# Kernel optimization log

Measured on AMD Instinct MI355X. Metric: run time of the kernel, lower is better.

Reference implementation:

```python
import jax, jax.numpy as jnp
import numpy as np

B, V, H = 4, 256, 128
EPS = 1e-5


def setup_inputs() -> dict:
    key = jax.random.key(0)
    ks = jax.random.split(key, 16)
    inp = {
        "h1": jax.random.normal(ks[0], (B, V, H), jnp.float32),
        "h2": jax.random.normal(ks[1], (B, V, H), jnp.float32),
        "e": jax.random.normal(ks[2], (B, V, V, H), jnp.float32),
        "graph": jax.random.randint(ks[3], (B, V, V), 0, 2, jnp.int32),
    }
    scale = 1.0 / np.sqrt(H)
    for i, nm in enumerate(["U1", "U2", "V1", "V2", "A1", "A2", "C"]):
        inp[f"W_{nm}"] = jax.random.normal(ks[4 + i], (H, H), jnp.float32) * scale
        inp[f"b_{nm}"] = jnp.zeros((H,), jnp.float32)
    for nm in ["h1", "h2", "e"]:
        inp[f"g_{nm}"] = jnp.ones((H,), jnp.float32)   # BN gamma
        inp[f"be_{nm}"] = jnp.zeros((H,), jnp.float32)  # BN beta
    return inp


def _lin(x, W, b):
    # torch nn.Linear: x @ W.T + b
    return jnp.einsum('...i,oi->...o', x, W) + b


def _bn(x, g, b):
    # BatchNorm1d with track_running_stats=False: batch stats over flattened leading dims
    sh = x.shape
    x2 = x.reshape(-1, sh[-1])
    m = x2.mean(axis=0)
    v = x2.var(axis=0)  # biased, as torch BN uses for normalization
    return ((x2 - m) * jax.lax.rsqrt(v + EPS) * g + b).reshape(sh)


def reference(h1, h2, e, graph,
              W_U1, b_U1, W_U2, b_U2, W_V1, b_V1, W_V2, b_V2,
              W_A1, b_A1, W_A2, b_A2, W_C, b_C,
              g_h1, be_h1, g_h2, be_h2, g_e, be_e):
    h1_in, h2_in, e_in = h1, h2, e

    Uh1 = _lin(h1, W_U1, b_U1)
    Uh2 = _lin(h2, W_U2, b_U2)
    Vh1 = _lin(h1, W_V1, b_V1)
    Vh2 = _lin(h2, W_V2, b_V2)

    # Wh1[b,i,j,h] = Vh1[b,j,h] + Vh2[b,i,h] ; Wh2 = transpose(1,2) pattern
    Wh1 = Vh1[:, None, :, :] + Vh2[:, :, None, :]
    Wh2 = Vh1[:, :, None, :] + Vh2[:, None, :, :]

    Ah1 = _lin(h1, W_A1, b_A1)
    Ah2 = _lin(h2, W_A2, b_A2)
    Ce = _lin(e, W_C, b_C)
    e_new = Ah1[:, None, :, :] + Ah2[:, :, None, :] + Ce  # B x V x V x H

    gates = jax.nn.sigmoid(e_new)
    gates_T = jax.nn.sigmoid(jnp.transpose(e_new, (0, 2, 1, 3)))

    # aggregation = 'sum' over dim 2 (graph unused for sum)
    h1n = Uh1 + jnp.sum(gates * Wh1, axis=2)
    h2n = Uh2 + jnp.sum(gates_T * Wh2, axis=2)

    h1n = jax.nn.relu(_bn(h1n, g_h1, be_h1))
    h2n = jax.nn.relu(_bn(h2n, g_h2, be_h2))
    e_out = jax.nn.relu(_bn(e_new, g_e, be_e))

    # mode == 'residual'
    return (h1_in + h1n, h2_in + h2n, e_in + e_out)
```

## Files before the change

### kernel.cpp

```cpp
#include <hip/hip_runtime.h>
#include <math.h>

#define BB 4
#define VV 256
#define HH 128
#define EPS 1e-5f

typedef __attribute__((ext_vector_type(8))) short short8;
typedef __attribute__((ext_vector_type(8))) __bf16 bf16x8;
typedef __attribute__((ext_vector_type(4))) float f32x4;

__device__ __forceinline__ float sigm_(float x) {
    return 1.0f / (1.0f + __expf(-x));
}

__device__ __forceinline__ bf16x8 as_bf(short8 s) {
    union { short8 s; bf16x8 b; } u; u.s = s; return u.b;
}

__device__ __forceinline__ void split8n(const float4 x0, const float4 x1,
                                        bf16x8& hi, bf16x8& lo) {
    float xs[8] = {x0.x, x0.y, x0.z, x0.w, x1.x, x1.y, x1.z, x1.w};
    #pragma unroll
    for (int i = 0; i < 8; ++i) {
        float x = xs[i];
        __bf16 h = (__bf16)x;
        float r = x - (float)h;
        hi[i] = h;
        lo[i] = (__bf16)r;
    }
}

__global__ __launch_bounds__(256) void k0_splitW(const float* __restrict__ W_C,
                                                 short* __restrict__ Whl) {
    int t = blockIdx.x * 256 + threadIdx.x;
    int lane = t & 63;
    int grp = t >> 6;
    int kstep = grp >> 3, nsub = grp & 7;
    int n = nsub * 16 + (lane & 15);
    int kb = kstep * 32 + ((lane >> 4) & 3) * 8;
    const float4* src = (const float4*)(W_C + (size_t)n * HH + kb);
    float4 x0 = src[0], x1 = src[1];
    bf16x8 hi, lo;
    split8n(x0, x1, hi, lo);
    union { bf16x8 b; short8 s; } uh, ul;
    uh.b = hi; ul.b = lo;
    short8* dst = (short8*)Whl;
    dst[(size_t)grp * 128 + 0 * 64 + lane] = uh.s;
    dst[(size_t)grp * 128 + 1 * 64 + lane] = ul.s;
}

struct LinArgs {
    const float* x1; const float* x2;
    const float* W[6]; const float* b[6]; const float* b2[6];
    float* out[6]; float* outf[6];
};

__global__ __launch_bounds__(128) void k1_linears(LinArgs a) {
    __shared__ float xs[2][8][HH];
    const int t = threadIdx.x;
    const int r0 = blockIdx.x * 8;
    {
        const float4* s1 = (const float4*)(a.x1 + (size_t)r0 * HH);
        const float4* s2 = (const float4*)(a.x2 + (size_t)r0 * HH);
        float4* d1 = (float4*)&xs[0][0][0];
        float4* d2 = (float4*)&xs[1][0][0];
        #pragma unroll
        for (int p = 0; p < 2; ++p) {
            d1[t + p * 128] = s1[t + p * 128];
            d2[t + p * 128] = s2[t + p * 128];
        }
    }
    __syncthreads();
    const int h = t;
    const int l15h = h & 15, nsh = h >> 4;
    for (int g = 0; g < 6; ++g) {
        const float* W = a.W[g];
        const float (*x)[HH] = (g < 3) ? xs[0] : xs[1];
        float acc[8];
        #pragma unroll
        for (int r = 0; r < 8; ++r) acc[r] = 0.f;
        const float4* Wrow = (const float4*)(W + (size_t)h * HH);
        #pragma unroll 8
        for (int kq = 0; kq < 32; ++kq) {
            float4 w4 = Wrow[kq];
            #pragma unroll
            for (int r = 0; r < 8; ++r) {
                float4 ev = *(const float4*)&x[r][kq * 4];
                acc[r] = fmaf(ev.x, w4.x, acc[r]);
                acc[r] = fmaf(ev.y, w4.y, acc[r]);
                acc[r] = fmaf(ev.z, w4.z, acc[r]);
                acc[r] = fmaf(ev.w, w4.w, acc[r]);
            }
        }
        float bias = a.b[g][h];
        if (a.b2[g]) bias += a.b2[g][h];
        if (a.out[g]) {
            float* O = a.out[g] + (size_t)r0 * HH + h;
            #pragma unroll
            for (int r = 0; r < 8; ++r) O[(size_t)r * HH] = acc[r] + bias;
        }
        if (a.outf[g]) {
            float* Of = a.outf[g];
            #pragma unroll
            for (int r = 0; r < 8; ++r)
                Of[((size_t)(r0 + r) * 16 + l15h) * 8 + nsh] = acc[r] + bias;
        }
    }
}

__global__ __launch_bounds__(512, 4) void k2_main(
    const float* __restrict__ e,
    const short* __restrict__ Whl,
    const float* __restrict__ A1f, const float* __restrict__ A2f,
    const float* __restrict__ V1f, const float* __restrict__ V2f,
    float* __restrict__ e_new,
    float* __restrict__ h1acc,
    float* __restrict__ stats)
{
    __shared__ short8 sW[4096];
    __shared__ float red[8][3][8][16];
    const int t = threadIdx.x;
    const int l = t & 63;
    const int w = t >> 6;
    const int l15 = l & 15;
    const int lq = (l >> 4) & 3;
    const int bi = blockIdx.x;
    const int b = bi >> 8;
    const int jbase = w * 32;

    {
        const short8* src = (const short8*)Whl;
        #pragma unroll
        for (int p = 0; p < 8; ++p) sW[p * 512 + t] = src[p * 512 + t];
    }
    __syncthreads();

    const float* ebase = e + (size_t)bi * (VV * HH);
    const float* pa = ebase + (size_t)(jbase + l15) * HH + lq * 8;

    f32x4 acc[2][8];
    #pragma unroll
    for (int js = 0; js < 2; ++js)
        #pragma unroll
        for (int ns = 0; ns < 8; ++ns)
            acc[js][ns] = (f32x4){0.f, 0.f, 0.f, 0.f};

    float4 ec0 = *(const float4*)(pa);
    float4 ec1 = *(const float4*)(pa + 4);
    float4 ec2 = *(const float4*)(pa + 16 * HH);
    float4 ec3 = *(const float4*)(pa + 16 * HH + 4);

    #pragma unroll
    for (int kstep = 0; kstep < 4; ++kstep) {
        bf16x8 ah[2], al[2];
        split8n(ec0, ec1, ah[0], al[0]);
        split8n(ec2, ec3, ah[1], al[1]);
        if (kstep < 3) {
            const float* pn = pa + (kstep + 1) * 32;
            ec0 = *(const float4*)(pn);
            ec1 = *(const float4*)(pn + 4);
            ec2 = *(const float4*)(pn + 16 * HH);
            ec3 = *(const float4*)(pn + 16 * HH + 4);
        }
        #pragma unroll
        for (int ns = 0; ns < 8; ++ns) {
            short8 bh = sW[(size_t)(kstep * 8 + ns) * 128 + l];
            short8 bl = sW[(size_t)(kstep * 8 + ns) * 128 + 64 + l];
            acc[0][ns] = __builtin_amdgcn_mfma_f32_16x16x32_bf16(
                ah[0], as_bf(bh), acc[0][ns], 0, 0, 0);
            acc[1][ns] = __builtin_amdgcn_mfma_f32_16x16x32_bf16(
                ah[1], as_bf(bh), acc[1][ns], 0, 0, 0);
            acc[0][ns] = __builtin_amdgcn_mfma_f32_16x16x32_bf16(
                ah[0], as_bf(bl), acc[0][ns], 0, 0, 0);
            acc[1][ns] = __builtin_amdgcn_mfma_f32_16x16x32_bf16(
                ah[1], as_bf(bl), acc[1][ns], 0, 0, 0);
            acc[0][ns] = __builtin_amdgcn_mfma_f32_16x16x32_bf16(
                al[0], as_bf(bh), acc[0][ns], 0, 0, 0);
            acc[1][ns] = __builtin_amdgcn_mfma_f32_16x16x32_bf16(
                al[1], as_bf(bh), acc[1][ns], 0, 0, 0);
        }
    }

    union f8u { float4 v[2]; float f[8]; };
    f8u a2, v2;
    {
        const float4* p = (const float4*)(A2f + ((size_t)bi * 16 + l15) * 8);
        a2.v[0] = p[0]; a2.v[1] = p[1];
        const float4* q = (const float4*)(V2f + ((size_t)bi * 16 + l15) * 8);
        v2.v[0] = q[0]; v2.v[1] = q[1];
    }
    float h1a[8], es[8], eq[8];
    #pragma unroll
    for (int ns = 0; ns < 8; ++ns) { h1a[ns] = 0.f; es[ns] = 0.f; eq[ns] = 0.f; }

    #pragma unroll
    for (int js = 0; js < 2; ++js) {
        #pragma unroll
        for (int r = 0; r < 4; ++r) {
            int j = jbase + js * 16 + lq * 4 + r;
            size_t fro = ((size_t)(b * VV + j) * 16 + l15) * 8;
            f8u a1, v1;
            {
                const float4* p = (const float4*)(A1f + fro);
                a1.v[0] = p[0]; a1.v[1] = p[1];
                const float4* q = (const float4*)(V1f + fro);
                v1.v[0] = q[0]; v1.v[1] = q[1];
            }
            size_t obase = ((size_t)bi * VV + j) * HH;
            #pragma unroll
            for (int ns = 0; ns < 8; ++ns) {
                float en = acc[js][ns][r] + a1.f[ns] + a2.f[ns];
                e_new[obase + ns * 16 + l15] = en;
                float s = sigm_(en);
                h1a[ns] = fmaf(s, v1.f[ns] + v2.f[ns], h1a[ns]);
                es[ns] += en;
                eq[ns] = fmaf(en, en, eq[ns]);
            }
        }
    }

    #pragma unroll
    for (int ns = 0; ns < 8; ++ns) {
        h1a[ns] += __shfl_xor(h1a[ns], 16);
        h1a[ns] += __shfl_xor(h1a[ns], 32);
        es[ns]  += __shfl_xor(es[ns], 16);
        es[ns]  += __shfl_xor(es[ns], 32);
        eq[ns]  += __shfl_xor(eq[ns], 16);
        eq[ns]  += __shfl_xor(eq[ns], 32);
    }
    if (l < 16) {
        #pragma unroll
        for (int ns = 0; ns < 8; ++ns) {
            red[w][0][ns][l15] = h1a[ns];
            red[w][1][ns][l15] = es[ns];
            red[w][2][ns][l15] = eq[ns];
        }
    }
    __syncthreads();
    if (t < 128) {
        int ns = t >> 4, li = t & 15;
        float h1t = 0.f, est = 0.f, eqt = 0.f;
        #pragma unroll
        for (int ww = 0; ww < 8; ++ww) {
            h1t += red[ww][0][ns][li];
            est += red[ww][1][ns][li];
            eqt += red[ww][2][ns][li];
        }
        int n = t;
        h1acc[(size_t)bi * HH + n] = h1t;
        atomicAdd(&stats[0 * HH + n], est);
        atomicAdd(&stats[1 * HH + n], eqt);
    }
}

__global__ __launch_bounds__(256) void k4_pass2(
    float* __restrict__ e_io,
    const float* __restrict__ e_in,
    const float* __restrict__ V1, const float* __restrict__ V2,
    const float* __restrict__ g_e, const float* __restrict__ be_e,
    float* __restrict__ h2acc,
    const float* __restrict__ stats)
{
    const int t = threadIdx.x;
    const int h4 = (t & 31) * 4;
    const int jsub = t >> 5;
    const int blk = blockIdx.x;
    const int Iq = blk & 7;
    const int Jt = (blk >> 3) & 31;
    const int b = blk >> 8;
    const int J = Jt * 8 + jsub;
    const int bJ = (b << 8) + J;

    const float inv_n = 1.0f / (float)(BB * VV * VV);
    float sc[4], sh[4];
    #pragma unroll
    for (int c = 0; c < 4; ++c) {
        int h = h4 + c;
        float mean = stats[0 * HH + h] * inv_n;
        float var  = stats[1 * HH + h] * inv_n - mean * mean;
        float rstd = rsqrtf(var + EPS);
        sc[c] = rstd * g_e[h];
        sh[c] = be_e[h] - mean * sc[c];
    }
    float4 vh1 = *(const float4*)(V1 + (size_t)bJ * HH + h4);
    float4 h2a = {0.f, 0.f, 0.f, 0.f};

    const int I0beg = Iq * 32;
    for (int I0 = I0beg; I0 < I0beg + 32; I0 += 4) {
        float4 en[4], ei[4], v2[4];
        size_t off[4];
        #pragma unroll
        for (int u = 0; u < 4; ++u) {
            int I = I0 + u;
            off[u] = ((size_t)((b * VV + I) * VV) + J) * HH + h4;
            en[u] = *(const float4*)(e_io + off[u]);
            ei[u] = *(const float4*)(e_in + off[u]);
            v2[u] = *(const float4*)(V2 + (size_t)((b << 8) + I) * HH + h4);
        }
        #pragma unroll
        for (int u = 0; u < 4; ++u) {
            float4 r;
            float* enf = (float*)&en[u];
            float* eif = (float*)&ei[u];
            float* v2f = (float*)&v2[u];
            float* rf = (float*)&r;
            float* h2f = (float*)&h2a;
            float* v1f = (float*)&vh1;
            #pragma unroll
            for (int c = 0; c < 4; ++c) {
                float e_ = enf[c];
                h2f[c] = fmaf(sigm_(e_), v1f[c] + v2f[c], h2f[c]);
                float bn = fmaf(e_, sc[c], sh[c]);
                rf[c] = eif[c] + fmaxf(bn, 0.f);
            }
            *(float4*)(e_io + off[u]) = r;
        }
    }
    float* base = h2acc + (size_t)bJ * HH + h4;
    float* h2f = (float*)&h2a;
    #pragma unroll
    for (int c = 0; c < 4; ++c) atomicAdd(base + c, h2f[c]);
}

__global__ __launch_bounds__(256) void k45_combine(
    float* __restrict__ h1acc, float* __restrict__ h2acc,
    const float* __restrict__ U1, const float* __restrict__ U2,
    float* __restrict__ stats)
{
    __shared__ float red[2][2][128];
    const int t = threadIdx.x;
    const int h = t & 127;
    const int rr = t >> 7;
    const int region = blockIdx.x >> 5;
    const int r0 = (blockIdx.x & 31) * 32;
    float* acc = region ? h2acc : h1acc;
    const float* U = region ? U2 : U1;
    float s = 0.f, q = 0.f;
    #pragma unroll
    for (int rs = 0; rs < 16; ++rs) {
        size_t idx = (size_t)(r0 + rr * 16 + rs) * HH + h;
        float v = acc[idx] + U[idx];
        acc[idx] = v;
        s += v;
        q = fmaf(v, v, q);
    }
    red[0][rr][h] = s;
    red[1][rr][h] = q;
    __syncthreads();
    if (t < 128) {
        atomicAdd(&stats[(2 + 2 * region) * HH + h], red[0][0][h] + red[0][1][h]);
        atomicAdd(&stats[(3 + 2 * region) * HH + h], red[1][0][h] + red[1][1][h]);
    }
}

__global__ __launch_bounds__(256) void k5_final(
    const float* __restrict__ h1_in, const float* __restrict__ h2_in,
    const float* __restrict__ h1p, const float* __restrict__ h2p,
    const float* __restrict__ g1, const float* __restrict__ be1,
    const float* __restrict__ g2, const float* __restrict__ be2,
    float* __restrict__ out,
    const float* __restrict__ stats)
{
    const float inv_n = 1.0f / 1024.0f;
    int idx0 = blockIdx.x * 2048 + threadIdx.x;
    #pragma unroll
    for (int p = 0; p < 8; ++p) {
        int idx = idx0 + p * 256;
        int region = idx >> 17;
        int local = idx & 131071;
        int h = idx & 127;
        float ssum = stats[(2 + 2 * region) * HH + h];
        float ssq  = stats[(3 + 2 * region) * HH + h];
        float mean = ssum * inv_n;
        float var  = ssq * inv_n - mean * mean;
        float rstd = rsqrtf(var + EPS);
        const float* g  = region ? g2 : g1;
        const float* be = region ? be2 : be1;
        float sc = rstd * g[h];
        float sh = be[h] - mean * sc;
        const float* xin = region ? h2_in : h1_in;
        const float* pre = region ? h2p : h1p;
        out[idx] = xin[local] + fmaxf(fmaf(pre[local], sc, sh), 0.f);
    }
}

extern "C" void kernel_launch(void* const* d_in, const int* in_sizes, int n_in,
                              void* d_out, int out_size, void* d_ws, size_t ws_size,
                              hipStream_t stream) {
    const float* h1   = (const float*)d_in[0];
    const float* h2   = (const float*)d_in[1];
    const float* e    = (const float*)d_in[2];
    const float* W_U1 = (const float*)d_in[4];
    const float* b_U1 = (const float*)d_in[5];
    const float* W_U2 = (const float*)d_in[6];
    const float* b_U2 = (const float*)d_in[7];
    const float* W_V1 = (const float*)d_in[8];
    const float* b_V1 = (const float*)d_in[9];
    const float* W_V2 = (const float*)d_in[10];
    const float* b_V2 = (const float*)d_in[11];
    const float* W_A1 = (const float*)d_in[12];
    const float* b_A1 = (const float*)d_in[13];
    const float* W_A2 = (const float*)d_in[14];
    const float* b_A2 = (const float*)d_in[15];
    const float* W_C  = (const float*)d_in[16];
    const float* b_C  = (const float*)d_in[17];
    const float* g_h1 = (const float*)d_in[18];
    const float* be_h1= (const float*)d_in[19];
    const float* g_h2 = (const float*)d_in[20];
    const float* be_h2= (const float*)d_in[21];
    const float* g_e  = (const float*)d_in[22];
    const float* be_e = (const float*)d_in[23];

    float* ws = (float*)d_ws;
    const size_t S = (size_t)BB * VV * HH;
    float* U1  = ws + 0 * S;
    float* U2  = ws + 1 * S;
    float* V1  = ws + 2 * S;
    float* V2  = ws + 3 * S;
    float* V1f = ws + 4 * S;
    float* V2f = ws + 5 * S;
    float* A1f = ws + 6 * S;
    float* A2f = ws + 7 * S;
    float* h1acc = ws + 8 * S;
    float* h2acc = ws + 9 * S;
    float* stats = ws + 10 * S;
    short* Whl  = (short*)(stats + 768);

    float* out = (float*)d_out;
    float* eo = out + 2 * S;

    hipMemsetAsync(h1acc, 0, (2 * S + 768) * sizeof(float), stream);

    k0_splitW<<<8, 256, 0, stream>>>(W_C, Whl);

    LinArgs la;
    la.x1 = h1; la.x2 = h2;
    la.W[0] = W_U1; la.b[0] = b_U1; la.b2[0] = nullptr; la.out[0] = U1; la.outf[0] = nullptr;
    la.W[1] = W_V1; la.b[1] = b_V1; la.b2[1] = nullptr; la.out[1] = V1; la.outf[1] = V1f;
    la.W[2] = W_A1; la.b[2] = b_A1; la.b2[2] = b_C;     la.out[2] = nullptr; la.outf[2] = A1f;
    la.W[3] = W_U2; la.b[3] = b_U2; la.b2[3] = nullptr; la.out[3] = U2; la.outf[3] = nullptr;
    la.W[4] = W_V2; la.b[4] = b_V2; la.b2[4] = nullptr; la.out[4] = V2; la.outf[4] = V2f;
    la.W[5] = W_A2; la.b[5] = b_A2; la.b2[5] = nullptr; la.out[5] = nullptr; la.outf[5] = A2f;
    k1_linears<<<128, 128, 0, stream>>>(la);

    k2_main<<<BB * VV, 512, 0, stream>>>(e, Whl, A1f, A2f, V1f, V2f,
                                         eo, h1acc, stats);

    k4_pass2<<<BB * 32 * 8, 256, 0, stream>>>(eo, e, V1, V2, g_e, be_e,
                                              h2acc, stats);

    k45_combine<<<64, 256, 0, stream>>>(h1acc, h2acc, U1, U2, stats);

    k5_final<<<128, 256, 0, stream>>>(h1, h2, h1acc, h2acc,
                                      g_h1, be_h1, g_h2, be_h2, out, stats);
}
```

Baseline: 200.3 us.

## Swap MFMA operand order for row-contiguous float4 e_new stores

Swaps the A/B operands of the bf16 MFMA so each lane's accumulator holds four consecutive H columns instead of four rows. The epilogue can then write e_new and read A1/V1 in row-major layout as float4 vectors, and the fragment-ordered copies V1f/V2f/A1f/A2f produced by the linear kernel are dropped. The reduction changes from cross-quadrant shuffles to 16-lane xor shuffles per column group, with a flat shared buffer. This cuts scattered scalar global stores and workspace traffic, at the cost of more shuffle steps and loop-varying register indexing.

Result: slower. 213.2 us (+6.5%).

```diff
diff --git a/kernel.cpp b/kernel.cpp
--- a/kernel.cpp
+++ b/kernel.cpp
@@ -53,7 +53,7 @@
 struct LinArgs {
     const float* x1; const float* x2;
     const float* W[6]; const float* b[6]; const float* b2[6];
-    float* out[6]; float* outf[6];
+    float* out[6];
 };
 
 __global__ __launch_bounds__(128) void k1_linears(LinArgs a) {
@@ -73,7 +73,6 @@
     }
     __syncthreads();
     const int h = t;
-    const int l15h = h & 15, nsh = h >> 4;
     for (int g = 0; g < 6; ++g) {
         const float* W = a.W[g];
         const float (*x)[HH] = (g < 3) ? xs[0] : xs[1];
@@ -95,31 +94,24 @@
         }
         float bias = a.b[g][h];
         if (a.b2[g]) bias += a.b2[g][h];
-        if (a.out[g]) {
-            float* O = a.out[g] + (size_t)r0 * HH + h;
-            #pragma unroll
-            for (int r = 0; r < 8; ++r) O[(size_t)r * HH] = acc[r] + bias;
-        }
-        if (a.outf[g]) {
-            float* Of = a.outf[g];
-            #pragma unroll
-            for (int r = 0; r < 8; ++r)
-                Of[((size_t)(r0 + r) * 16 + l15h) * 8 + nsh] = acc[r] + bias;
-        }
+        float* O = a.out[g] + (size_t)r0 * HH + h;
+        #pragma unroll
+        for (int r = 0; r < 8; ++r) O[(size_t)r * HH] = acc[r] + bias;
     }
 }
 
 __global__ __launch_bounds__(512, 4) void k2_main(
     const float* __restrict__ e,
     const short* __restrict__ Whl,
-    const float* __restrict__ A1f, const float* __restrict__ A2f,
-    const float* __restrict__ V1f, const float* __restrict__ V2f,
+    const float* __restrict__ A1b,
+    const float* __restrict__ A2,
+    const float* __restrict__ V1, const float* __restrict__ V2,
     float* __restrict__ e_new,
     float* __restrict__ h1acc,
     float* __restrict__ stats)
 {
     __shared__ short8 sW[4096];
-    __shared__ float red[8][3][8][16];
+    __shared__ float red[8][3][128];
     const int t = threadIdx.x;
     const int l = t & 63;
     const int w = t >> 6;
@@ -168,89 +160,81 @@
             short8 bh = sW[(size_t)(kstep * 8 + ns) * 128 + l];
             short8 bl = sW[(size_t)(kstep * 8 + ns) * 128 + 64 + l];
             acc[0][ns] = __builtin_amdgcn_mfma_f32_16x16x32_bf16(
-                ah[0], as_bf(bh), acc[0][ns], 0, 0, 0);
+                as_bf(bh), ah[0], acc[0][ns], 0, 0, 0);
             acc[1][ns] = __builtin_amdgcn_mfma_f32_16x16x32_bf16(
-                ah[1], as_bf(bh), acc[1][ns], 0, 0, 0);
+                as_bf(bh), ah[1], acc[1][ns], 0, 0, 0);
             acc[0][ns] = __builtin_amdgcn_mfma_f32_16x16x32_bf16(
-                ah[0], as_bf(bl), acc[0][ns], 0, 0, 0);
+                as_bf(bl), ah[0], acc[0][ns], 0, 0, 0);
             acc[1][ns] = __builtin_amdgcn_mfma_f32_16x16x32_bf16(
-                ah[1], as_bf(bl), acc[1][ns], 0, 0, 0);
+                as_bf(bl), ah[1], acc[1][ns], 0, 0, 0);
             acc[0][ns] = __builtin_amdgcn_mfma_f32_16x16x32_bf16(
-                al[0], as_bf(bh), acc[0][ns], 0, 0, 0);
+                as_bf(bh), al[0], acc[0][ns], 0, 0, 0);
             acc[1][ns] = __builtin_amdgcn_mfma_f32_16x16x32_bf16(
-                al[1], as_bf(bh), acc[1][ns], 0, 0, 0);
-        }
-    }
-
-    union f8u { float4 v[2]; float f[8]; };
-    f8u a2, v2;
-    {
-        const float4* p = (const float4*)(A2f + ((size_t)bi * 16 + l15) * 8);
-        a2.v[0] = p[0]; a2.v[1] = p[1];
-        const float4* q = (const float4*)(V2f + ((size_t)bi * 16 + l15) * 8);
-        v2.v[0] = q[0]; v2.v[1] = q[1];
-    }
-    float h1a[8], es[8], eq[8];
-    #pragma unroll
-    for (int ns = 0; ns < 8; ++ns) { h1a[ns] = 0.f; es[ns] = 0.f; eq[ns] = 0.f; }
-
-    #pragma unroll
-    for (int js = 0; js < 2; ++js) {
-        #pragma unroll
-        for (int r = 0; r < 4; ++r) {
-            int j = jbase + js * 16 + lq * 4 + r;
-            size_t fro = ((size_t)(b * VV + j) * 16 + l15) * 8;
-            f8u a1, v1;
-            {
-                const float4* p = (const float4*)(A1f + fro);
-                a1.v[0] = p[0]; a1.v[1] = p[1];
-                const float4* q = (const float4*)(V1f + fro);
-                v1.v[0] = q[0]; v1.v[1] = q[1];
+                as_bf(bh), al[1], acc[1][ns], 0, 0, 0);
+        }
+    }
+
+    #pragma unroll
+    for (int ns = 0; ns < 8; ++ns) {
+        const int nbase = ns * 16 + lq * 4;
+        float4 a2q = *(const float4*)(A2 + (size_t)bi * HH + nbase);
+        float4 v2q = *(const float4*)(V2 + (size_t)bi * HH + nbase);
+        f32x4 h1a = {0.f, 0.f, 0.f, 0.f};
+        f32x4 es  = {0.f, 0.f, 0.f, 0.f};
+        f32x4 eq  = {0.f, 0.f, 0.f, 0.f};
+        #pragma unroll
+        for (int js = 0; js < 2; ++js) {
+            const int j = jbase + js * 16 + l15;
+            const size_t ra = (size_t)(b * VV + j) * HH + nbase;
+            float4 a1 = *(const float4*)(A1b + ra);
+            float4 v1 = *(const float4*)(V1 + ra);
+            float4 en4;
+            const float* a1f = (const float*)&a1;
+            const float* v1f = (const float*)&v1;
+            const float* a2f = (const float*)&a2q;
+            const float* v2f = (const float*)&v2q;
+            float* enf = (float*)&en4;
+            #pragma unroll
+            for (int r = 0; r < 4; ++r) {
+                float en = acc[js][ns][r] + a1f[r] + a2f[r];
+                enf[r] = en;
+                float s = sigm_(en);
+                h1a[r] = fmaf(s, v1f[r] + v2f[r], h1a[r]);
+                es[r] += en;
+                eq[r] = fmaf(en, en, eq[r]);
             }
-            size_t obase = ((size_t)bi * VV + j) * HH;
+            *(float4*)(e_new + ((size_t)bi * VV + j) * HH + nbase) = en4;
+        }
+        #pragma unroll
+        for (int m = 1; m < 16; m <<= 1) {
             #pragma unroll
-            for (int ns = 0; ns < 8; ++ns) {
-                float en = acc[js][ns][r] + a1.f[ns] + a2.f[ns];
-                e_new[obase + ns * 16 + l15] = en;
-                float s = sigm_(en);
-                h1a[ns] = fmaf(s, v1.f[ns] + v2.f[ns], h1a[ns]);
-                es[ns] += en;
-                eq[ns] = fmaf(en, en, eq[ns]);
+            for (int r = 0; r < 4; ++r) {
+                h1a[r] += __shfl_xor(h1a[r], m);
+                es[r]  += __shfl_xor(es[r], m);
+                eq[r]  += __shfl_xor(eq[r], m);
             }
         }
-    }
-
-    #pragma unroll
-    for (int ns = 0; ns < 8; ++ns) {
-        h1a[ns] += __shfl_xor(h1a[ns], 16);
-        h1a[ns] += __shfl_xor(h1a[ns], 32);
-        es[ns]  += __shfl_xor(es[ns], 16);
-        es[ns]  += __shfl_xor(es[ns], 32);
-        eq[ns]  += __shfl_xor(eq[ns], 16);
-        eq[ns]  += __shfl_xor(eq[ns], 32);
-    }
-    if (l < 16) {
-        #pragma unroll
-        for (int ns = 0; ns < 8; ++ns) {
-            red[w][0][ns][l15] = h1a[ns];
-            red[w][1][ns][l15] = es[ns];
-            red[w][2][ns][l15] = eq[ns];
+        if (l15 == 0) {
+            #pragma unroll
+            for (int r = 0; r < 4; ++r) {
+                red[w][0][nbase + r] = h1a[r];
+                red[w][1][nbase + r] = es[r];
+                red[w][2][nbase + r] = eq[r];
+            }
         }
     }
     __syncthreads();
     if (t < 128) {
-        int ns = t >> 4, li = t & 15;
         float h1t = 0.f, est = 0.f, eqt = 0.f;
         #pragma unroll
         for (int ww = 0; ww < 8; ++ww) {
-            h1t += red[ww][0][ns][li];
-            est += red[ww][1][ns][li];
-            eqt += red[ww][2][ns][li];
-        }
-        int n = t;
-        h1acc[(size_t)bi * HH + n] = h1t;
-        atomicAdd(&stats[0 * HH + n], est);
-        atomicAdd(&stats[1 * HH + n], eqt);
+            h1t += red[ww][0][t];
+            est += red[ww][1][t];
+            eqt += red[ww][2][t];
+        }
+        h1acc[(size_t)bi * HH + t] = h1t;
+        atomicAdd(&stats[0 * HH + t], est);
+        atomicAdd(&stats[1 * HH + t], eqt);
     }
 }
 
@@ -418,33 +402,31 @@
     float* U2  = ws + 1 * S;
     float* V1  = ws + 2 * S;
     float* V2  = ws + 3 * S;
-    float* V1f = ws + 4 * S;
-    float* V2f = ws + 5 * S;
-    float* A1f = ws + 6 * S;
-    float* A2f = ws + 7 * S;
-    float* h1acc = ws + 8 * S;
-    float* h2acc = ws + 9 * S;
-    float* stats = ws + 10 * S;
+    float* A1b = ws + 4 * S;
+    float* A2  = ws + 5 * S;
+    float* h1acc = ws + 6 * S;
+    float* h2acc = ws + 7 * S;
+    float* stats = ws + 8 * S;
     short* Whl  = (short*)(stats + 768);
 
     float* out = (float*)d_out;
     float* eo = out + 2 * S;
 
-    hipMemsetAsync(h1acc, 0, (2 * S + 768) * sizeof(float), stream);
+    hipMemsetAsync(h2acc, 0, (S + 768) * sizeof(float), stream);
 
     k0_splitW<<<8, 256, 0, stream>>>(W_C, Whl);
 
     LinArgs la;
     la.x1 = h1; la.x2 = h2;
-    la.W[0] = W_U1; la.b[0] = b_U1; la.b2[0] = nullptr; la.out[0] = U1; la.outf[0] = nullptr;
-    la.W[1] = W_V1; la.b[1] = b_V1; la.b2[1] = nullptr; la.out[1] = V1; la.outf[1] = V1f;
-    la.W[2] = W_A1; la.b[2] = b_A1; la.b2[2] = b_C;     la.out[2] = nullptr; la.outf[2] = A1f;
-    la.W[3] = W_U2; la.b[3] = b_U2; la.b2[3] = nullptr; la.out[3] = U2; la.outf[3] = nullptr;
-    la.W[4] = W_V2; la.b[4] = b_V2; la.b2[4] = nullptr; la.out[4] = V2; la.outf[4] = V2f;
-    la.W[5] = W_A2; la.b[5] = b_A2; la.b2[5] = nullptr; la.out[5] = nullptr; la.outf[5] = A2f;
+    la.W[0] = W_U1; la.b[0] = b_U1; la.b2[0] = nullptr; la.out[0] = U1;
+    la.W[1] = W_V1; la.b[1] = b_V1; la.b2[1] = nullptr; la.out[1] = V1;
+    la.W[2] = W_A1; la.b[2] = b_A1; la.b2[2] = b_C;     la.out[2] = A1b;
+    la.W[3] = W_U2; la.b[3] = b_U2; la.b2[3] = nullptr; la.out[3] = U2;
+    la.W[4] = W_V2; la.b[4] = b_V2; la.b2[4] = nullptr; la.out[4] = V2;
+    la.W[5] = W_A2; la.b[5] = b_A2; la.b2[5] = nullptr; la.out[5] = A2;
     k1_linears<<<128, 128, 0, stream>>>(la);
 
-    k2_main<<<BB * VV, 512, 0, stream>>>(e, Whl, A1f, A2f, V1f, V2f,
+    k2_main<<<BB * VV, 512, 0, stream>>>(e, Whl, A1b, A2, V1, V2,
                                          eo, h1acc, stats);
 
     k4_pass2<<<BB * 32 * 8, 256, 0, stream>>>(eo, e, V1, V2, g_e, be_e,
```
